# Kernel optimization log

Hardware: AMD Instinct MI355X
Metric: run time of the kernel (lower is better)

The kernel has to match this reference:

```python
import math
import jax, jax.numpy as jnp
import numpy as np

B, S, H, NH = 8, 1024, 1024, 16
HD = H // NH  # head dim = 64

def setup_inputs() -> dict:
    key = jax.random.key(0)
    ks = jax.random.split(key, 4)
    scale = 1.0 / math.sqrt(H)
    return {
        "hidden_state": jax.random.normal(ks[0], (B, S, H), jnp.float32),
        "attention_mask": jnp.ones((B, 1, S), jnp.float32),
        "Wq": jax.random.normal(ks[1], (H, H), jnp.float32) * scale,
        "bq": jnp.zeros((H,), jnp.float32),
        "Wk": jax.random.normal(ks[2], (H, H), jnp.float32) * scale,
        "bk": jnp.zeros((H,), jnp.float32),
        "Wv": jax.random.normal(ks[3], (H, H), jnp.float32) * scale,
        "bv": jnp.zeros((H,), jnp.float32),
    }

def _split_heads(x):
    # [B,S,H] -> [B,NH,S,HD]
    return x.reshape(B, S, NH, HD).transpose(0, 2, 1, 3)

def reference(hidden_state, attention_mask, Wq, bq, Wk, bk, Wv, bv):
    q = _split_heads(hidden_state @ Wq.T + bq)
    k = _split_heads(hidden_state @ Wk.T + bk)
    v = _split_heads(hidden_state @ Wv.T + bv)
    scores = jnp.einsum("bhqd,bhkd->bhqk", q, k) / math.sqrt(HD)
    # mask [B,1,S] -> additive bias [B,1,S,1], broadcast over heads and keys
    bias = (1.0 - attention_mask)[..., None] * -10000.0
    scores = scores + bias
    probs = jax.nn.softmax(scores, axis=-1)  # dropout prob = 0.0 (eval)
    ctx = jnp.einsum("bhqk,bhkd->bhqd", probs, v)
    return ctx.transpose(0, 2, 1, 3).reshape(B, S, H)
```

## Files before the change

kernel.cpp:

```cpp
#include <hip/hip_runtime.h>
#include <hip/hip_bf16.h>


typedef __attribute__((ext_vector_type(8))) short bf16x8;
typedef __attribute__((ext_vector_type(4))) float f32x4;
typedef unsigned short u16;

#define NB 8
#define NS 1024
#define NH_ 16
#define HD_ 64
#define QKV_T (NB * NH_ * NS * HD_)
#define XN (8192 * 1024)
#define WN (1024 * 1024)
#define QSCL 0.180336880f

static __device__ __forceinline__ u16 f2bf(float f) {
    unsigned int u = __float_as_uint(f);
    u += 0x7FFFu + ((u >> 16) & 1u);
    return (u16)(u >> 16);
}

static __device__ __forceinline__ bf16x8 cvt8(const float* p) {
    float4 a = *(const float4*)p;
    float4 b = *(const float4*)(p + 4);
    union { bf16x8 v; u16 s[8]; } r;
    r.s[0] = f2bf(a.x); r.s[1] = f2bf(a.y); r.s[2] = f2bf(a.z); r.s[3] = f2bf(a.w);
    r.s[4] = f2bf(b.x); r.s[5] = f2bf(b.y); r.s[6] = f2bf(b.z); r.s[7] = f2bf(b.w);
    return r.v;
}

static __device__ __forceinline__ void async16(const u16* g, u16* l) {
    __builtin_amdgcn_global_load_lds((const __attribute__((address_space(1))) void*)g,
                                     (__attribute__((address_space(3))) void*)l,
                                     16, 0, 0);
}

static __device__ __forceinline__ unsigned int cvtpk(float a, float b) {
    unsigned int r;
    asm("v_cvt_pk_bf16_f32 %0, %1, %2" : "=v"(r) : "v"(a), "v"(b));
    return r;
}

__global__ __launch_bounds__(256) void cvt_pass(
    const float* __restrict__ X,
    const float* __restrict__ Wq, const float* __restrict__ Wk,
    const float* __restrict__ Wv,
    u16* __restrict__ Xb, u16* __restrict__ Wb)
{
    size_t i8 = ((size_t)blockIdx.x * 256 + threadIdx.x) * 8;
    if (i8 < XN) {
        *(bf16x8*)(Xb + i8) = cvt8(X + i8);
    } else {
        size_t j = i8 - XN;
        int w = (int)(j >> 20);
        const float* src = (w == 0) ? Wq : (w == 1) ? Wk : Wv;
        *(bf16x8*)(Wb + j) = cvt8(src + (j & (WN - 1)));
    }
}

#define GEMM2_LDS_BYTES 131072

__global__ __launch_bounds__(512, 2) void qkv_gemm_8ph(
    const u16* __restrict__ Xb, const u16* __restrict__ Wb,
    const float* __restrict__ bq, const float* __restrict__ bk,
    const float* __restrict__ bv,
    u16* __restrict__ qkv)
{
    extern __shared__ u16 sm[];

    const int tid  = threadIdx.x;
    const int lane = tid & 63;
    const int wid  = tid >> 6;
    const int l15  = lane & 15;
    const int quad = lane >> 4;
    const int sw   = l15 & 7;
    const int wr   = wid >> 2;
    const int wc   = wid & 3;

    const int bid = blockIdx.x;
    const int xcd = bid & 7;
    const int loc = bid >> 3;
    const int m0  = ((xcd & 3) * 8 + loc / 6) * 256;
    const int n0  = ((xcd >> 2) * 6 + loc % 6) * 256;

    const u16* Ap = Xb + (size_t)m0 * 1024;
    const u16* Bp = Wb + (size_t)n0 * 1024;

    int offG[2], offL[2];
#pragma unroll
    for (int it = 0; it < 2; ++it) {
        int idx = it * 512 + tid;
        int lr = idx >> 3, kc = idx & 7;
        offG[it] = lr * 1024 + ((kc ^ (lr & 7)) * 8);
        offL[it] = idx * 8;
    }

    const int arow = wr * 64 + l15;
    const int brow = wc * 32 + l15;

    f32x4 acc[2][2][4][2];
#pragma unroll
    for (int qm = 0; qm < 2; ++qm)
#pragma unroll
        for (int qn = 0; qn < 2; ++qn)
#pragma unroll
            for (int mi = 0; mi < 4; ++mi)
#pragma unroll
                for (int ni = 0; ni < 2; ++ni)
                    acc[qm][qn][mi][ni] = (f32x4){0.f, 0.f, 0.f, 0.f};

    bf16x8 a[4][2], b[2][2];

#define STG_A(BUF, H, T) do { if ((T) < 16) { \
    _Pragma("unroll") for (int it = 0; it < 2; ++it) \
        async16(Ap + (size_t)(H) * 131072 + (T) * 64 + offG[it], \
                sm + ((BUF) * 4 + (H)) * 8192 + offL[it]); } } while (0)
#define STG_B(BUF, H, T) do { if ((T) < 16) { \
    _Pragma("unroll") for (int it = 0; it < 2; ++it) \
        async16(Bp + (size_t)(H) * 131072 + (T) * 64 + offG[it], \
                sm + ((BUF) * 4 + 2 + (H)) * 8192 + offL[it]); } } while (0)
#define LDA(BUF, QM) do { \
    _Pragma("unroll") for (int mi = 0; mi < 4; ++mi) { \
        _Pragma("unroll") for (int kk = 0; kk < 2; ++kk) \
            a[mi][kk] = *(const bf16x8*)&sm[((BUF) * 4 + (QM)) * 8192 + \
                (arow + mi * 16) * 64 + (((kk * 4 + quad) ^ sw) * 8)]; } } while (0)
#define LDB(BUF, QN) do { \
    _Pragma("unroll") for (int ni = 0; ni < 2; ++ni) { \
        _Pragma("unroll") for (int kk = 0; kk < 2; ++kk) \
            b[ni][kk] = *(const bf16x8*)&sm[((BUF) * 4 + 2 + (QN)) * 8192 + \
                (brow + ni * 16) * 64 + (((kk * 4 + quad) ^ sw) * 8)]; } } while (0)
#define MM(QM, QN) do { __builtin_amdgcn_s_setprio(1); \
    _Pragma("unroll") for (int kk = 0; kk < 2; ++kk) \
    _Pragma("unroll") for (int mi = 0; mi < 4; ++mi) \
    _Pragma("unroll") for (int ni = 0; ni < 2; ++ni) \
        acc[QM][QN][mi][ni] = __builtin_amdgcn_mfma_f32_16x16x32_bf16( \
            a[mi][kk], b[ni][kk], acc[QM][QN][mi][ni], 0, 0, 0); \
    __builtin_amdgcn_s_setprio(0); } while (0)
#define BAR asm volatile("s_barrier" ::: "memory")
#define WAITV4 asm volatile("s_waitcnt vmcnt(4)" ::: "memory")
#define WAITV0 asm volatile("s_waitcnt vmcnt(0)" ::: "memory")

    STG_A(0, 0, 0); STG_B(0, 1, 0); STG_A(0, 1, 0);
    STG_B(0, 0, 0); STG_A(1, 0, 1); STG_B(1, 1, 1);
    WAITV4;
    BAR;

    for (int jj = 0; jj < 8; ++jj) {
        const int j0 = jj * 2, j1 = j0 + 1;
        LDA(0, 0); LDB(0, 0); STG_A(1, 1, j0 + 1); MM(0, 0); BAR;
        LDB(0, 1);            STG_B(1, 0, j0 + 1); MM(0, 1); BAR;
        LDA(0, 1);            STG_A(0, 0, j0 + 2); MM(1, 1); BAR;
        LDB(0, 0);            STG_B(0, 1, j0 + 2); MM(1, 0);
        if (jj == 7) { WAITV0; } else { WAITV4; }
        BAR;
        LDA(1, 0); LDB(1, 0); STG_A(0, 1, j1 + 1); MM(0, 0); BAR;
        LDB(1, 1);            STG_B(0, 0, j1 + 1); MM(0, 1); BAR;
        LDA(1, 1);            STG_A(1, 0, j1 + 2); MM(1, 1); BAR;
        LDB(1, 0);            STG_B(1, 1, j1 + 2); MM(1, 0);
        if (jj < 7) { WAITV4; BAR; }
    }

    const int which = n0 >> 10;
    const int ncol0 = n0 & 1023;
    const int batch = m0 >> 10;
    const int mrow0 = m0 & 1023;
    const float* bias = (which == 0) ? bq : (which == 1) ? bk : bv;
    const float scl   = (which == 0) ? QSCL : 1.0f;

    if (which == 2) {
#pragma unroll
        for (int qm = 0; qm < 2; ++qm)
#pragma unroll
            for (int qn = 0; qn < 2; ++qn)
#pragma unroll
                for (int ni = 0; ni < 2; ++ni) {
                    int col = ncol0 + qn * 128 + wc * 32 + ni * 16 + l15;
                    float bia = bias[col];
                    int h = col >> 6;
                    int d = col & 63;
                    size_t base = (size_t)((2 * NB + batch) * NH_ + h) * (NS * HD_);
#pragma unroll
                    for (int mi = 0; mi < 4; ++mi) {
                        int s = mrow0 + qm * 128 + wr * 64 + mi * 16 + quad * 4;
                        ushort4 pk;
                        pk.x = f2bf(acc[qm][qn][mi][ni][0] + bia);
                        pk.y = f2bf(acc[qm][qn][mi][ni][1] + bia);
                        pk.z = f2bf(acc[qm][qn][mi][ni][2] + bia);
                        pk.w = f2bf(acc[qm][qn][mi][ni][3] + bia);
                        *(ushort4*)&qkv[base + (size_t)d * NS + s] = pk;
                    }
                }
    } else {
        u16* Cs = sm;
        const size_t tb = (size_t)((which * NB + batch) * NH_) * (NS * HD_);
        const int h0 = ncol0 >> 6;
        __syncthreads();
#pragma unroll
        for (int qm = 0; qm < 2; ++qm) {
            if (qm) __syncthreads();
#pragma unroll
            for (int qn = 0; qn < 2; ++qn)
#pragma unroll
                for (int ni = 0; ni < 2; ++ni) {
                    int col = qn * 128 + wc * 32 + ni * 16 + l15;
                    float bia = bias[ncol0 + col];
#pragma unroll
                    for (int mi = 0; mi < 4; ++mi)
#pragma unroll
                        for (int r = 0; r < 4; ++r)
                            Cs[(wr * 64 + mi * 16 + quad * 4 + r) * 264 + col] =
                                f2bf((acc[qm][qn][mi][ni][r] + bia) * scl);
                }
            __syncthreads();
#pragma unroll
            for (int it = 0; it < 8; ++it) {
                int idx = it * 512 + tid;
                int lr = idx >> 5;
                int c  = idx & 31;
                int s  = mrow0 + qm * 128 + lr;
                int h  = h0 + (c >> 3);
                *(uint4*)&qkv[tb + (size_t)h * (NS * HD_) + (size_t)s * HD_ + (c & 7) * 8] =
                    *(const uint4*)&Cs[lr * 264 + c * 8];
            }
        }
    }
#undef STG_A
#undef STG_B
#undef LDA
#undef LDB
#undef MM
#undef BAR
#undef WAITV4
#undef WAITV0
}

__global__ __launch_bounds__(256) void qkv_gemm_f32(
    const float* __restrict__ X,
    const float* __restrict__ Wq, const float* __restrict__ bq,
    const float* __restrict__ Wk, const float* __restrict__ bk,
    const float* __restrict__ Wv, const float* __restrict__ bv,
    u16* __restrict__ qkv)
{
    __shared__ u16 As[128 * 72];
    __shared__ u16 Bs[128 * 72];
    const int tid  = threadIdx.x;
    const int lane = tid & 63;
    const int wid  = tid >> 6;
    const int l15  = lane & 15;
    const int quad = lane >> 4;
    const int wm   = (wid >> 1) * 64;
    const int wn   = (wid & 1) * 64;
    const int m0   = blockIdx.x * 128;
    const int nb   = blockIdx.y * 128;
    const int which = nb >> 10;
    const int ncol0 = nb & 1023;
    const float* W    = (which == 0) ? Wq : (which == 1) ? Wk : Wv;
    const float* bias = (which == 0) ? bq : (which == 1) ? bk : bv;
    const float scl   = (which == 0) ? QSCL : 1.0f;

    f32x4 acc[4][4];
#pragma unroll
    for (int mi = 0; mi < 4; ++mi)
#pragma unroll
        for (int ni = 0; ni < 4; ++ni) acc[mi][ni] = (f32x4){0.f, 0.f, 0.f, 0.f};

    for (int kt = 0; kt < 16; ++kt) {
#pragma unroll
        for (int it = 0; it < 4; ++it) {
            int idx = it * 256 + tid;
            int row = idx >> 3, c = idx & 7;
            *(bf16x8*)&As[row * 72 + c * 8] = cvt8(&X[(size_t)(m0 + row) * 1024 + kt * 64 + c * 8]);
            *(bf16x8*)&Bs[row * 72 + c * 8] = cvt8(&W[(size_t)(ncol0 + row) * 1024 + kt * 64 + c * 8]);
        }
        __syncthreads();
#pragma unroll
        for (int kk = 0; kk < 2; ++kk) {
            bf16x8 a[4], b[4];
#pragma unroll
            for (int mi = 0; mi < 4; ++mi)
                a[mi] = *(const bf16x8*)&As[(wm + mi * 16 + l15) * 72 + kk * 32 + quad * 8];
#pragma unroll
            for (int ni = 0; ni < 4; ++ni)
                b[ni] = *(const bf16x8*)&Bs[(wn + ni * 16 + l15) * 72 + kk * 32 + quad * 8];
#pragma unroll
            for (int mi = 0; mi < 4; ++mi)
#pragma unroll
                for (int ni = 0; ni < 4; ++ni)
                    acc[mi][ni] = __builtin_amdgcn_mfma_f32_16x16x32_bf16(
                        a[mi], b[ni], acc[mi][ni], 0, 0, 0);
        }
        __syncthreads();
    }
#pragma unroll
    for (int ni = 0; ni < 4; ++ni) {
        int nn = ncol0 + wn + ni * 16 + l15;
        float bia = bias[nn];
        int h = nn >> 6;
        int d = nn & 63;
#pragma unroll
        for (int mi = 0; mi < 4; ++mi) {
#pragma unroll
            for (int r = 0; r < 4; ++r) {
                int rg    = m0 + wm + mi * 16 + quad * 4 + r;
                int batch = rg >> 10;
                int s     = rg & 1023;
                size_t base = (size_t)((which * NB + batch) * NH_ + h) * (NS * HD_);
                size_t off  = (which == 2) ? base + (size_t)d * NS + s
                                           : base + (size_t)s * HD_ + d;
                qkv[off] = f2bf((acc[mi][ni][r] + bia) * scl);
            }
        }
    }
}

__global__ __launch_bounds__(256) void attn(
    const u16* __restrict__ qkv, float* __restrict__ out)
{
    __shared__ u16 Ks[2][64 * 64];
    __shared__ u16 VTs[2][64 * 64];
    __shared__ u16 Ps[128 * 72];

    const int tid  = threadIdx.x;
    const int lane = tid & 63;
    const int wid  = tid >> 6;
    const int l15  = lane & 15;
    const int quad = lane >> 4;
    const int sw   = l15 & 7;

    const int id    = blockIdx.x;
    const int hb    = (id & 7) * 16 + ((id >> 3) >> 3);
    const int q0    = ((id >> 3) & 7) * 128;
    const int h     = hb & 15;
    const int batch = hb >> 4;

    const size_t headoff = (size_t)(batch * NH_ + h) * (NS * HD_);
    const u16* Qg = qkv + headoff;
    const u16* Kg = qkv + (size_t)QKV_T + headoff;
    const u16* Vt = qkv + (size_t)2 * QKV_T + headoff;

    const u16* kp[2];
    const u16* vp[2];
#pragma unroll
    for (int it = 0; it < 2; ++it) {
        int idx = it * 256 + tid;
        int row = idx >> 3, kc = idx & 7;
        int kcs = (kc ^ (row & 7)) * 8;
        kp[it] = Kg + (size_t)row * 64 + kcs;
        vp[it] = Vt + (size_t)row * NS + kcs;
    }

    bf16x8 aq[2][2];
#pragma unroll
    for (int f = 0; f < 2; ++f)
#pragma unroll
        for (int kk = 0; kk < 2; ++kk)
            aq[f][kk] = *(const bf16x8*)&Qg[(size_t)(q0 + wid * 32 + f * 16 + l15) * 64 + kk * 32 + quad * 8];

#pragma unroll
    for (int it = 0; it < 2; ++it) {
        int idx = it * 256 + tid;
        async16(kp[it], Ks[0] + idx * 8);
        async16(vp[it], VTs[0] + idx * 8);
    }
    __syncthreads();

    float lsum[2] = {0.f, 0.f};
    f32x4 o[2][4];
#pragma unroll
    for (int f = 0; f < 2; ++f)
#pragma unroll
        for (int ni = 0; ni < 4; ++ni) o[f][ni] = (f32x4){0.f, 0.f, 0.f, 0.f};

    for (int kt = 0; kt < 16; ++kt) {
        const u16* Kc = Ks[kt & 1];
        const u16* Vc = VTs[kt & 1];

        if (kt < 15) {
            u16* Kn = Ks[(kt & 1) ^ 1];
            u16* Vn = VTs[(kt & 1) ^ 1];
#pragma unroll
            for (int it = 0; it < 2; ++it) {
                int idx = it * 256 + tid;
                async16(kp[it] + (size_t)(kt + 1) * 4096, Kn + idx * 8);
                async16(vp[it] + (size_t)(kt + 1) * 64, Vn + idx * 8);
            }
        }

        f32x4 sfr[2][4];
        __builtin_amdgcn_s_setprio(1);
#pragma unroll
        for (int ni = 0; ni < 4; ++ni) {
            bf16x8 b0 = *(const bf16x8*)&Kc[(ni * 16 + l15) * 64 + ((quad ^ sw) * 8)];
            bf16x8 b1 = *(const bf16x8*)&Kc[(ni * 16 + l15) * 64 + (((4 + quad) ^ sw) * 8)];
#pragma unroll
            for (int f = 0; f < 2; ++f) {
                f32x4 sa = (f32x4){0.f, 0.f, 0.f, 0.f};
                sa = __builtin_amdgcn_mfma_f32_16x16x32_bf16(b0, aq[f][0], sa, 0, 0, 0);
                sa = __builtin_amdgcn_mfma_f32_16x16x32_bf16(b1, aq[f][1], sa, 0, 0, 0);
                sfr[f][ni] = sa;
            }
        }
        __builtin_amdgcn_s_setprio(0);

#pragma unroll
        for (int f = 0; f < 2; ++f)
#pragma unroll
            for (int ni = 0; ni < 4; ++ni) {
                float p0 = __builtin_amdgcn_exp2f(sfr[f][ni][0]);
                float p1 = __builtin_amdgcn_exp2f(sfr[f][ni][1]);
                float p2 = __builtin_amdgcn_exp2f(sfr[f][ni][2]);
                float p3 = __builtin_amdgcn_exp2f(sfr[f][ni][3]);
                lsum[f] += (p0 + p1) + (p2 + p3);
                uint2 pk;
                pk.x = cvtpk(p0, p1);
                pk.y = cvtpk(p2, p3);
                *(uint2*)&Ps[(wid * 32 + f * 16 + l15) * 72 + ni * 16 + quad * 4] = pk;
            }

        __builtin_amdgcn_s_setprio(1);
#pragma unroll
        for (int kk = 0; kk < 2; ++kk) {
            bf16x8 ap[2];
#pragma unroll
            for (int f = 0; f < 2; ++f)
                ap[f] = *(const bf16x8*)&Ps[(wid * 32 + f * 16 + l15) * 72 + kk * 32 + quad * 8];
#pragma unroll
            for (int ni = 0; ni < 4; ++ni) {
                bf16x8 bv_ = *(const bf16x8*)&Vc[(ni * 16 + l15) * 64 + (((kk * 4 + quad) ^ sw) * 8)];
#pragma unroll
                for (int f = 0; f < 2; ++f)
                    o[f][ni] = __builtin_amdgcn_mfma_f32_16x16x32_bf16(ap[f], bv_, o[f][ni], 0, 0, 0);
            }
        }
        __builtin_amdgcn_s_setprio(0);
        __syncthreads();
    }

#pragma unroll
    for (int f = 0; f < 2; ++f) {
        lsum[f] += __shfl_xor(lsum[f], 16, 64);
        lsum[f] += __shfl_xor(lsum[f], 32, 64);
    }

#pragma unroll
    for (int f = 0; f < 2; ++f) {
        float inv[4];
#pragma unroll
        for (int r = 0; r < 4; ++r)
            inv[r] = 1.0f / __shfl(lsum[f], quad * 4 + r, 64);
#pragma unroll
        for (int ni = 0; ni < 4; ++ni)
#pragma unroll
            for (int r = 0; r < 4; ++r) {
                int row = wid * 32 + f * 16 + quad * 4 + r;
                out[(size_t)(batch * NS + q0 + row) * 1024 + h * 64 + ni * 16 + l15] =
                    o[f][ni][r] * inv[r];
            }
    }
}

extern "C" void kernel_launch(void* const* d_in, const int* in_sizes, int n_in,
                              void* d_out, int out_size, void* d_ws, size_t ws_size,
                              hipStream_t stream) {
    const float* X  = (const float*)d_in[0];
    const float* Wq = (const float*)d_in[2];
    const float* bq = (const float*)d_in[3];
    const float* Wk = (const float*)d_in[4];
    const float* bk = (const float*)d_in[5];
    const float* Wv = (const float*)d_in[6];
    const float* bv = (const float*)d_in[7];
    float* outp = (float*)d_out;

    u16* qkv = (u16*)d_ws;
    u16* Xb  = (u16*)((char*)d_ws + (size_t)QKV_T * 3 * 2);
    u16* Wb  = Xb + XN;
    const size_t need = (size_t)QKV_T * 3 * 2 + (size_t)XN * 2 + (size_t)3 * WN * 2;

    static bool attr_done = false;
    if (!attr_done) {
        (void)hipFuncSetAttribute((const void*)qkv_gemm_8ph,
                                  hipFuncAttributeMaxDynamicSharedMemorySize,
                                  GEMM2_LDS_BYTES);
        attr_done = true;
    }

    if (ws_size >= need) {
        cvt_pass<<<(XN + 3 * WN) / 8 / 256, 256, 0, stream>>>(X, Wq, Wk, Wv, Xb, Wb);
        qkv_gemm_8ph<<<384, 512, GEMM2_LDS_BYTES, stream>>>(Xb, Wb, bq, bk, bv, qkv);
    } else {
        qkv_gemm_f32<<<dim3(64, 24), 256, 0, stream>>>(X, Wq, bq, Wk, bk, Wv, bv, qkv);
    }
    attn<<<1024, 256, 0, stream>>>(qkv, outp);
}
```

Before: 222.5 us.

## Double attention block to 256 queries with 8 waves sharing K/V tiles

The attention kernel now runs 512 threads per block, covering 256 query rows instead of 128. The K/V tile loads are split across twice as many threads, so each thread issues one async copy per tile instead of two. This halves the number of blocks and the redundant K/V global traffic per head. In exchange it uses dynamic shared memory with a larger Ps buffer and sets launch bounds of 512 with min 4 blocks, which could pressure registers and occupancy.

```diff
diff --git a/kernel.cpp b/kernel.cpp
--- a/kernel.cpp
+++ b/kernel.cpp
@@ -314,12 +314,15 @@
     }
 }
 
-__global__ __launch_bounds__(256) void attn(
+#define ATTN_LDS_BYTES 69632
+
+__global__ __launch_bounds__(512, 4) void attn(
     const u16* __restrict__ qkv, float* __restrict__ out)
 {
-    __shared__ u16 Ks[2][64 * 64];
-    __shared__ u16 VTs[2][64 * 64];
-    __shared__ u16 Ps[128 * 72];
+    extern __shared__ u16 asm_[];
+    u16* KsB  = asm_;
+    u16* VTsB = asm_ + 8192;
+    u16* Ps   = asm_ + 16384;
 
     const int tid  = threadIdx.x;
     const int lane = tid & 63;
@@ -329,8 +332,8 @@
     const int sw   = l15 & 7;
 
     const int id    = blockIdx.x;
-    const int hb    = (id & 7) * 16 + ((id >> 3) >> 3);
-    const int q0    = ((id >> 3) & 7) * 128;
+    const int hb    = (id & 7) * 16 + (id >> 5);
+    const int q0    = ((id >> 3) & 3) * 256;
     const int h     = hb & 15;
     const int batch = hb >> 4;
 
@@ -339,16 +342,12 @@
     const u16* Kg = qkv + (size_t)QKV_T + headoff;
     const u16* Vt = qkv + (size_t)2 * QKV_T + headoff;
 
-    const u16* kp[2];
-    const u16* vp[2];
-#pragma unroll
-    for (int it = 0; it < 2; ++it) {
-        int idx = it * 256 + tid;
-        int row = idx >> 3, kc = idx & 7;
-        int kcs = (kc ^ (row & 7)) * 8;
-        kp[it] = Kg + (size_t)row * 64 + kcs;
-        vp[it] = Vt + (size_t)row * NS + kcs;
-    }
+    {
+    }
+    const int srow = tid >> 3, skc = tid & 7;
+    const int skcs = (skc ^ (srow & 7)) * 8;
+    const u16* kp = Kg + (size_t)srow * 64 + skcs;
+    const u16* vp = Vt + (size_t)srow * NS + skcs;
 
     bf16x8 aq[2][2];
 #pragma unroll
@@ -357,12 +356,8 @@
         for (int kk = 0; kk < 2; ++kk)
             aq[f][kk] = *(const bf16x8*)&Qg[(size_t)(q0 + wid * 32 + f * 16 + l15) * 64 + kk * 32 + quad * 8];
 
-#pragma unroll
-    for (int it = 0; it < 2; ++it) {
-        int idx = it * 256 + tid;
-        async16(kp[it], Ks[0] + idx * 8);
-        async16(vp[it], VTs[0] + idx * 8);
-    }
+    async16(kp, KsB + tid * 8);
+    async16(vp, VTsB + tid * 8);
     __syncthreads();
 
     float lsum[2] = {0.f, 0.f};
@@ -373,18 +368,14 @@
         for (int ni = 0; ni < 4; ++ni) o[f][ni] = (f32x4){0.f, 0.f, 0.f, 0.f};
 
     for (int kt = 0; kt < 16; ++kt) {
-        const u16* Kc = Ks[kt & 1];
-        const u16* Vc = VTs[kt & 1];
+        const u16* Kc = KsB + (kt & 1) * 4096;
+        const u16* Vc = VTsB + (kt & 1) * 4096;
 
         if (kt < 15) {
-            u16* Kn = Ks[(kt & 1) ^ 1];
-            u16* Vn = VTs[(kt & 1) ^ 1];
-#pragma unroll
-            for (int it = 0; it < 2; ++it) {
-                int idx = it * 256 + tid;
-                async16(kp[it] + (size_t)(kt + 1) * 4096, Kn + idx * 8);
-                async16(vp[it] + (size_t)(kt + 1) * 64, Vn + idx * 8);
-            }
+            u16* Kn = KsB + ((kt & 1) ^ 1) * 4096;
+            u16* Vn = VTsB + ((kt & 1) ^ 1) * 4096;
+            async16(kp + (size_t)(kt + 1) * 4096, Kn + tid * 8);
+            async16(vp + (size_t)(kt + 1) * 64, Vn + tid * 8);
         }
 
         f32x4 sfr[2][4];
@@ -482,6 +473,9 @@
         (void)hipFuncSetAttribute((const void*)qkv_gemm_8ph,
                                   hipFuncAttributeMaxDynamicSharedMemorySize,
                                   GEMM2_LDS_BYTES);
+        (void)hipFuncSetAttribute((const void*)attn,
+                                  hipFuncAttributeMaxDynamicSharedMemorySize,
+                                  ATTN_LDS_BYTES);
         attr_done = true;
     }
 
@@ -491,5 +485,5 @@
     } else {
         qkv_gemm_f32<<<dim3(64, 24), 256, 0, stream>>>(X, Wq, bq, Wk, bk, Wv, bv, qkv);
     }
-    attn<<<1024, 256, 0, stream>>>(qkv, outp);
-}
+    attn<<<512, 512, ATTN_LDS_BYTES, stream>>>(qkv, outp);
+}
```

After: 200.9 us. 9.7% less time.
